# Optimization experiments

Hardware: AMD Instinct MI355X
Metric: run time of the kernel (lower is better)

Reference implementation:

```python
import jax, jax.numpy as jnp
import numpy as np

D_IN = 1024
D_OUT = 1024

def setup_inputs() -> dict:
    key = jax.random.key(0)
    kx, kq, kk, kv = jax.random.split(key, 4)
    X = jax.random.normal(kx, (4, 2048, D_IN), dtype=jnp.float32)
    s = 1.0 / np.sqrt(D_IN)
    Wq = jax.random.uniform(kq, (D_IN, D_OUT), jnp.float32, -s, s)
    Wk = jax.random.uniform(kk, (D_IN, D_OUT), jnp.float32, -s, s)
    Wv = jax.random.uniform(kv, (D_IN, D_OUT), jnp.float32, -s, s)
    return {"X": X, "Wq": Wq, "Wk": Wk, "Wv": Wv}

def reference(X, Wq, Wk, Wv):
    # X: [b, s, d_in]; W*: [d_in, d_out] (torch Linear weight transposed)
    B, S, _ = X.shape
    q = jnp.einsum('bsd,de->bse', X, Wq)
    k = jnp.einsum('bsd,de->bse', X, Wk)
    v = jnp.einsum('bsd,de->bse', X, Wv)
    scores = jnp.einsum('bqe,bke->bqk', q, k)  # [b, s, s]
    causal = jnp.triu(jnp.ones((S, S), dtype=bool), k=1)
    scores = jnp.where(causal, -jnp.inf, scores)
    weights = jax.nn.softmax(scores / jnp.sqrt(jnp.asarray(k.shape[-1], scores.dtype)), axis=-1)
    # dropout p=0.0 (eval) -> identity
    return jnp.einsum('bqk,bke->bqe', weights, v)
```

## Files before the change

### kernel.cpp

```cpp
#include <hip/hip_runtime.h>
#include <cstdint>
#include <cmath>

typedef unsigned short u16;
typedef u16   u16x4  __attribute__((ext_vector_type(4)));
typedef u16   u16x8  __attribute__((ext_vector_type(8)));
typedef __bf16 bf16x8 __attribute__((ext_vector_type(8)));
typedef float f32x4  __attribute__((ext_vector_type(4)));

__device__ __forceinline__ u16 f2bf(float f) {
    uint32_t u = __builtin_bit_cast(uint32_t, f);
    u += 0x7fffu + ((u >> 16) & 1u);
    return (u16)(u >> 16);
}
__device__ __forceinline__ float bf2f(u16 v) {
    uint32_t u = ((uint32_t)v) << 16;
    return __builtin_bit_cast(float, u);
}
__device__ __forceinline__ void gload_lds16(const u16* g, u16* l) {
    __builtin_amdgcn_global_load_lds((const __attribute__((address_space(1))) void*)g,
                                     (__attribute__((address_space(3))) void*)l,
                                     16, 0, 0);
}

__global__ __launch_bounds__(256) void prep_kernel(const float* __restrict__ X,
                                                   const float* __restrict__ Wq,
                                                   const float* __restrict__ Wk,
                                                   const float* __restrict__ Wv,
                                                   u16* __restrict__ Xb,
                                                   u16* __restrict__ Wt) {
    __shared__ u16 tile[64 * 72];
    typedef float f4 __attribute__((ext_vector_type(4)));
    const int bid = blockIdx.x;
    if (bid < 8192) {
        const int idx = bid * 256 + threadIdx.x;
        f4 f = ((const f4*)X)[idx];
        u16x4 o;
        o[0] = f2bf(f[0]); o[1] = f2bf(f[1]); o[2] = f2bf(f[2]); o[3] = f2bf(f[3]);
        ((u16x4*)Xb)[idx] = o;
        return;
    }
    const int id = bid - 8192;
    const int z = id >> 8, rem = id & 255;
    const float* W = (z == 0) ? Wq : (z == 1) ? Wk : Wv;
    u16* out = Wt + ((size_t)z << 20);
    const int nt = (rem & 15) * 64, kt = (rem >> 4) * 64;
    const int t = threadIdx.x, r = t >> 2, cq = (t & 3) * 16;
    const float* src = W + (size_t)(kt + r) * 1024 + nt + cq;
#pragma unroll
    for (int q = 0; q < 4; q++) {
        f4 f = ((const f4*)src)[q];
        tile[r * 72 + cq + q * 4 + 0] = f2bf(f[0]);
        tile[r * 72 + cq + q * 4 + 1] = f2bf(f[1]);
        tile[r * 72 + cq + q * 4 + 2] = f2bf(f[2]);
        tile[r * 72 + cq + q * 4 + 3] = f2bf(f[3]);
    }
    __syncthreads();
    u16x8 o0, o1;
#pragma unroll
    for (int e = 0; e < 8; e++) { o0[e] = tile[(cq + e) * 72 + r]; o1[e] = tile[(cq + 8 + e) * 72 + r]; }
    u16* dst = out + (size_t)(nt + r) * 1024 + kt + cq;
    *(u16x8*)dst = o0;
    *(u16x8*)(dst + 8) = o1;
}

template <int OUTMODE>
__device__ __forceinline__ void gemm_bt_core(u16* __restrict__ smem,
                                             const u16* __restrict__ A,
                                             const u16* __restrict__ Bt,
                                             void* __restrict__ outp,
                                             const int ldk, const int ldo,
                                             const int kbeg, const int kend,
                                             const int m0, const int n0,
                                             const int om0, const int on0) {
    u16* As = smem;
    u16* Bs = smem + 4096;
    const int tid = (int)threadIdx.x;
    const int wave = tid >> 6, lane = tid & 63;
    const int wm = wave >> 1, wn = wave & 1;

    f32x4 acc[4][4] = {};

    const int sr = lane >> 2;
    const int scw = ((lane & 3) ^ ((sr >> 1) & 3)) * 8;
    const u16* gA = A  + (size_t)(m0 + wave * 32 + sr) * ldk + scw;
    const u16* gB = Bt + (size_t)(n0 + wave * 32 + sr) * ldk + scw;
    u16* lA = As + wave * 1024;
    u16* lB = Bs + wave * 1024;
    const size_t rstep = (size_t)ldk * 16;

    const int arow = lane & 15;
    const int ksw  = (arow >> 1) & 3;
    const int koff = (((lane >> 4) ^ ksw)) * 8;
    const u16* pa = As + (wm * 64 + arow) * 32 + koff;
    const u16* pb = Bs + (wn * 64 + arow) * 32 + koff;

    for (int k0 = kbeg; k0 < kend; k0 += 32) {
        gload_lds16(gA + k0,         lA);
        gload_lds16(gA + k0 + rstep, lA + 512);
        gload_lds16(gB + k0,         lB);
        gload_lds16(gB + k0 + rstep, lB + 512);
        __syncthreads();
        bf16x8 a[4], b[4];
#pragma unroll
        for (int i = 0; i < 4; i++) a[i] = *(const bf16x8*)(pa + i * 512);
#pragma unroll
        for (int j = 0; j < 4; j++) b[j] = *(const bf16x8*)(pb + j * 512);
#pragma unroll
        for (int i = 0; i < 4; i++)
#pragma unroll
            for (int j = 0; j < 4; j++)
                acc[i][j] = __builtin_amdgcn_mfma_f32_16x16x32_bf16(a[i], b[j], acc[i][j], 0, 0, 0);
        __syncthreads();
    }

    const int row0 = om0 + wm * 64 + ((lane >> 4) << 2);
    const int col0 = on0 + wn * 64 + (lane & 15);
    if constexpr (OUTMODE == 0) {
        u16* o = (u16*)outp;
#pragma unroll
        for (int i = 0; i < 4; i++)
#pragma unroll
            for (int r = 0; r < 4; r++) {
                u16* po = o + (size_t)(row0 + i * 16 + r) * ldo + col0;
#pragma unroll
                for (int j = 0; j < 4; j++) po[j * 16] = f2bf(acc[i][j][r]);
            }
    } else {
        float* o = (float*)outp;
#pragma unroll
        for (int i = 0; i < 4; i++)
#pragma unroll
            for (int r = 0; r < 4; r++) {
                float* po = o + (size_t)(row0 + i * 16 + r) * ldo + col0;
#pragma unroll
                for (int j = 0; j < 4; j++) po[j * 16] = acc[i][j][r];
            }
    }
}

__global__ __launch_bounds__(512, 2) void qkv_gemm_kernel(const u16* __restrict__ Xb,
                                                          const u16* __restrict__ Wt,
                                                          u16* __restrict__ QKV) {
    __shared__ u16 lds[49152];
    const int bid = blockIdx.x;
    const int xcd = bid & 7, slot = bid >> 3;
    const int z = slot >> 5, r32 = slot & 31;
    const int m0 = (xcd * 4 + (r32 >> 3)) << 8;
    const int n0 = (r32 & 7) << 7;

    const u16* __restrict__ A = Xb;
    const u16* __restrict__ B = Wt + ((size_t)z << 20);
    u16* __restrict__ C = QKV + ((size_t)z << 23);

    const int tid = (int)threadIdx.x;
    const int w = tid >> 6, l = tid & 63;
    const int wm = w >> 2, wn = w & 3;

    const int srow = w * 16 + (l >> 3);
    const int scol = ((l & 7) ^ ((l >> 3) & 7)) * 8;
    const u16* gA = A + (size_t)(m0 + srow) * 1024 + scol;
    const u16* gB = B + (size_t)(n0 + srow) * 1024 + scol;
    u16* const sA = lds + w * 1024;
    u16* const sB = lds + 32768 + w * 1024;

    const int c0 = ((l >> 4) ^ (l & 7)) * 8;
    const u16* const pa_ = lds + (wm * 64 + (l & 15)) * 64;
    const u16* const pb_ = lds + 32768 + (wn * 32 + (l & 15)) * 64;

    f32x4 acc[2][4][2] = {};
    bf16x8 a[4][2], b[2][2];

#define MFMA_ __builtin_amdgcn_mfma_f32_16x16x32_bf16
#define STG_A(BUF, H, T) \
    gload_lds16(gA + (size_t)((H) * 128) * 1024 + (T) * 64,       sA + (BUF) + (H) * 8192); \
    gload_lds16(gA + (size_t)((H) * 128 + 8) * 1024 + (T) * 64,   sA + (BUF) + (H) * 8192 + 512);
#define STG_B(BUF, T) \
    gload_lds16(gB + (T) * 64,                                    sB + ((BUF) >> 1)); \
    gload_lds16(gB + (size_t)8 * 1024 + (T) * 64,                 sB + ((BUF) >> 1) + 512);
#define LD_A(BUF, QA) \
    _Pragma("unroll") for (int m_ = 0; m_ < 4; m_++) { \
        a[m_][0] = *(const bf16x8*)(pa_ + (BUF) + (QA) * 8192 + m_ * 1024 + c0); \
        a[m_][1] = *(const bf16x8*)(pa_ + (BUF) + (QA) * 8192 + m_ * 1024 + (c0 ^ 32)); \
    }
#define LD_B(BUF) \
    _Pragma("unroll") for (int n_ = 0; n_ < 2; n_++) { \
        b[n_][0] = *(const bf16x8*)(pb_ + ((BUF) >> 1) + n_ * 1024 + c0); \
        b[n_][1] = *(const bf16x8*)(pb_ + ((BUF) >> 1) + n_ * 1024 + (c0 ^ 32)); \
    }
#define MM(QA) \
    _Pragma("unroll") for (int m_ = 0; m_ < 4; m_++) { \
        _Pragma("unroll") for (int n_ = 0; n_ < 2; n_++) { \
            acc[QA][m_][n_] = MFMA_(a[m_][0], b[n_][0], acc[QA][m_][n_], 0, 0, 0); \
            acc[QA][m_][n_] = MFMA_(a[m_][1], b[n_][1], acc[QA][m_][n_], 0, 0, 0); \
        } \
    }
#define VM6 asm volatile("s_waitcnt vmcnt(6)" ::: "memory");
#define VM2 asm volatile("s_waitcnt vmcnt(2)" ::: "memory");
#define VM0 asm volatile("s_waitcnt vmcnt(0)" ::: "memory");
#define VMN
#define BAR __builtin_amdgcn_s_barrier();
#define PRIO1 __builtin_amdgcn_s_setprio(1);
#define PRIO0 __builtin_amdgcn_s_setprio(0);
#define TILE(BUF, OBUF, T1, S1, T2, S2, VMA, VMB) \
    LD_A(BUF, 0) LD_B(BUF) \
    if (S1) { STG_A(OBUF, 1, T1) } \
    VMA BAR PRIO1 MM(0) PRIO0 BAR \
    LD_A(BUF, 1) \
    if (S2) { STG_A(BUF, 0, T2) STG_B(BUF, T2) } \
    VMB BAR PRIO1 MM(1) PRIO0 BAR

    STG_A(0, 0, 0) STG_B(0, 0) STG_A(0, 1, 0)
    STG_A(16384, 0, 1) STG_B(16384, 1)
    asm volatile("s_waitcnt vmcnt(6)" ::: "memory");
    __builtin_amdgcn_s_barrier();

#pragma unroll 1
    for (int i = 0; i < 7; ++i) {
        const int t1 = 2 * i + 1, t2 = 2 * i + 2, t3 = 2 * i + 3;
        TILE(0,     16384, t1, 1, t2, 1, VM6, VM6)
        TILE(16384, 0,     t2, 1, t3, 1, VM6, VM6)
    }
    TILE(0,     16384, 15, 1, 0, 0, VM6, VM2)
    TILE(16384, 0,     0,  0, 0, 0, VM0, VMN)

    const int row0 = m0 + wm * 64 + ((l >> 4) << 2);
    const int col0 = n0 + wn * 32 + (l & 15);
#pragma unroll
    for (int qa = 0; qa < 2; qa++)
#pragma unroll
        for (int m = 0; m < 4; m++)
#pragma unroll
            for (int r = 0; r < 4; r++) {
                u16* po = C + (size_t)(row0 + qa * 128 + m * 16 + r) * 1024 + col0;
#pragma unroll
                for (int n = 0; n < 2; n++) po[n * 16] = f2bf(acc[qa][m][n][r]);
            }
#undef MFMA_
#undef STG_A
#undef STG_B
#undef LD_A
#undef LD_B
#undef MM
#undef VM6
#undef VM2
#undef VM0
#undef VMN
#undef BAR
#undef PRIO1
#undef PRIO0
#undef TILE
}

__global__ __launch_bounds__(256) void s_tr_kernel(const u16* __restrict__ QKV,
                                                   u16* __restrict__ S,
                                                   u16* __restrict__ Vt) {
    __shared__ u16 smem[8192];
    const int bid = blockIdx.x;
    if (bid < 576) {
        const int xcd = bid & 7, slot = bid >> 3;
        const int b = xcd >> 1, half = xcd & 1;
        int it = half ? 11 : 0;
        const int ntiles = half ? 70 : 66;
        if (slot >= ntiles) return;
        int acc = 0;
        while (acc + it + 1 <= slot) { acc += it + 1; it++; }
        const int jt = slot - acc;
        const u16* Q  = QKV + ((size_t)b << 21);
        const u16* Kp = QKV + ((size_t)1 << 23) + ((size_t)b << 21);
        gemm_bt_core<0>(smem, Q, Kp, S + ((size_t)b << 22), 1024, 2048, 0, 1024,
                        it * 128, jt * 128, it * 128, jt * 128);
        return;
    }
    const int id = bid - 576;
    const int z = id >> 9, rem = id & 511;
    const u16* src = QKV + ((size_t)2 << 23) + ((size_t)z << 21);
    u16* dst = Vt + ((size_t)z << 21);
    const int st = (rem & 31) * 64, et = (rem >> 5) * 64;
    u16 (*tile)[72] = (u16(*)[72])smem;
    const int t = threadIdx.x, r = t >> 2, cq = (t & 3) * 16;
    const u16* p = src + (size_t)(st + r) * 1024 + et + cq;
    u16x8 u0 = *(const u16x8*)p;
    u16x8 u1 = *(const u16x8*)(p + 8);
#pragma unroll
    for (int e = 0; e < 8; e++) { tile[r][cq + e] = u0[e]; tile[r][cq + 8 + e] = u1[e]; }
    __syncthreads();
    u16x8 o0, o1;
#pragma unroll
    for (int e = 0; e < 8; e++) { o0[e] = tile[cq + e][r]; o1[e] = tile[cq + 8 + e][r]; }
    u16* q = dst + (size_t)(et + r) * 2048 + st + cq;
    *(u16x8*)q = o0;
    *(u16x8*)(q + 8) = o1;
}

__global__ __launch_bounds__(256) void pv_gemm_kernel(const u16* __restrict__ P,
                                                      const u16* __restrict__ Vt,
                                                      float* __restrict__ O,
                                                      float* __restrict__ Part) {
    __shared__ u16 smem[8192];
    const unsigned char IT[24]   = {15,14, 7,14,13,13,12,12, 15, 6,11,11,10,10, 9, 5,  0, 1, 2, 8, 3, 9, 8, 4};
    const unsigned char KIND[24] = { 1, 1, 0, 2, 1, 2, 1, 2,  2, 0, 1, 2, 1, 2, 1, 0,  0, 0, 0, 2, 0, 2, 1, 0};
    const int j = blockIdx.x;
    const int slot = j >> 5, combo = j & 31;
    const int it = IT[slot], kind = KIND[slot];
    const int b = combo >> 3, n0 = (combo & 7) * 128;
    const int u = it + 1, h = (u + 1) >> 1;
    const int k_lo = (kind == 2) ? h * 128 : 0;
    const int k_hi = (kind == 1) ? h * 128 : u * 128;
    if (kind == 2) {
        float* dst = Part + ((size_t)((it - 8) * 32 + combo) << 14);
        gemm_bt_core<1>(smem, P + ((size_t)b << 22), Vt + ((size_t)b << 21), dst,
                        2048, 128, k_lo, k_hi, it * 128, n0, 0, 0);
    } else {
        gemm_bt_core<1>(smem, P + ((size_t)b << 22), Vt + ((size_t)b << 21),
                        O + ((size_t)b << 21),
                        2048, 1024, k_lo, k_hi, it * 128, n0, it * 128, n0);
    }
}

__global__ __launch_bounds__(256) void reduce_kernel(float* __restrict__ O,
                                                     const float* __restrict__ Part) {
    const int t = blockIdx.x;
    const int tile = t >> 2, q = t & 3;
    const int it = 8 + (tile >> 5), combo = tile & 31;
    const int b = combo >> 3, n0 = (combo & 7) * 128;
    const f32x4* p = (const f32x4*)(Part + ((size_t)tile << 14)) + q * 1024;
    float* o = O + ((size_t)b << 21) + (size_t)(it * 128 + q * 32) * 1024 + n0;
    const int tid = threadIdx.x;
#pragma unroll
    for (int e = 0; e < 4; e++) {
        const int flat = e * 256 + tid;
        const int row = flat >> 5, col = (flat & 31) * 4;
        f32x4 pv = p[flat];
        f32x4* po = (f32x4*)(o + (size_t)row * 1024 + col);
        f32x4 ov = *po;
        ov[0] += pv[0]; ov[1] += pv[1]; ov[2] += pv[2]; ov[3] += pv[3];
        *po = ov;
    }
}

__global__ __launch_bounds__(256) void softmax_kernel(u16* __restrict__ S) {
    const int wave = threadIdx.x >> 6, lane = threadIdx.x & 63;
    const int g = blockIdx.x * 4 + wave;
    const int b = g >> 11, i = g & 2047;
    u16* row = S + ((size_t)b << 22) + ((size_t)i << 11);
    const int n = i + 1;
    const int kend = ((i >> 7) + 1) << 7;
    const int nt_ = (kend + 511) >> 9;
    const float NEG = -1e30f;
    float v[32];
    float m = NEG;
#pragma unroll
    for (int t = 0; t < 4; t++) {
        if (t < nt_) {
            u16x8 u = *(const u16x8*)(row + t * 512 + lane * 8);
#pragma unroll
            for (int e = 0; e < 8; e++) {
                const int col = t * 512 + lane * 8 + e;
                float f = (col < n) ? bf2f(u[e]) : NEG;
                v[t * 8 + e] = f;
                m = fmaxf(m, f);
            }
        }
    }
#pragma unroll
    for (int off = 32; off > 0; off >>= 1) m = fmaxf(m, __shfl_xor(m, off, 64));
    const float sc = 0.03125f * 1.44269504088896f;
    float s = 0.f;
#pragma unroll
    for (int t = 0; t < 4; t++) {
        if (t < nt_) {
#pragma unroll
            for (int e = 0; e < 8; e++) {
                const float x = v[t * 8 + e];
                const float e2 = (x == NEG) ? 0.f : exp2f((x - m) * sc);
                v[t * 8 + e] = e2;
                s += e2;
            }
        }
    }
#pragma unroll
    for (int off = 32; off > 0; off >>= 1) s += __shfl_xor(s, off, 64);
    const float inv = 1.f / s;
#pragma unroll
    for (int t = 0; t < 4; t++) {
        if (t < nt_) {
            u16x8 o;
#pragma unroll
            for (int e = 0; e < 8; e++) o[e] = f2bf(v[t * 8 + e] * inv);
            *(u16x8*)(row + t * 512 + lane * 8) = o;
        }
    }
}

extern "C" void kernel_launch(void* const* d_in, const int* in_sizes, int n_in,
                              void* d_out, int out_size, void* d_ws, size_t ws_size,
                              hipStream_t stream) {
    const float* X  = (const float*)d_in[0];
    const float* Wq = (const float*)d_in[1];
    const float* Wk = (const float*)d_in[2];
    const float* Wv = (const float*)d_in[3];
    float* out = (float*)d_out;

    u16* ws  = (u16*)d_ws;
    u16* Xb  = ws;
    u16* Wt  = Xb + ((size_t)1 << 23);
    u16* QKV = Wt + 3 * ((size_t)1 << 20);
    u16* S   = QKV + 3 * ((size_t)1 << 23);
    u16* Vt  = Xb;
    float* Part = (float*)QKV;

    prep_kernel<<<8960, 256, 0, stream>>>(X, Wq, Wk, Wv, Xb, Wt);
    qkv_gemm_kernel<<<768, 512, 0, stream>>>(Xb, Wt, QKV);
    s_tr_kernel<<<2624, 256, 0, stream>>>(QKV, S, Vt);
    softmax_kernel<<<2048, 256, 0, stream>>>(S);
    pv_gemm_kernel<<<768, 256, 0, stream>>>(S, Vt, out, Part);
    reduce_kernel<<<1024, 256, 0, stream>>>(out, Part);
}
```

Baseline: 237.6 us.

## Drop split-K partials and reduce kernel; pair short and long PV tiles

The PV GEMM no longer splits long causal row tiles into two K halves written to a partial buffer and summed by a separate reduce kernel. Each of 512 blocks now computes a full causal K range for one output tile. The grid is ordered so the first half covers short row tiles and the second half covers long ones in reverse, so a CU that finishes early picks up a long tile and per-CU work stays balanced. This removes the partial-buffer traffic and one kernel launch, but it relies on the dynamic block scheduler to actually pair short and long tiles.

```diff
diff --git a/kernel.cpp b/kernel.cpp
--- a/kernel.cpp
+++ b/kernel.cpp
@@ -295,48 +295,16 @@
 
 __global__ __launch_bounds__(256) void pv_gemm_kernel(const u16* __restrict__ P,
                                                       const u16* __restrict__ Vt,
-                                                      float* __restrict__ O,
-                                                      float* __restrict__ Part) {
+                                                      float* __restrict__ O) {
     __shared__ u16 smem[8192];
-    const unsigned char IT[24]   = {15,14, 7,14,13,13,12,12, 15, 6,11,11,10,10, 9, 5,  0, 1, 2, 8, 3, 9, 8, 4};
-    const unsigned char KIND[24] = { 1, 1, 0, 2, 1, 2, 1, 2,  2, 0, 1, 2, 1, 2, 1, 0,  0, 0, 0, 2, 0, 2, 1, 0};
     const int j = blockIdx.x;
-    const int slot = j >> 5, combo = j & 31;
-    const int it = IT[slot], kind = KIND[slot];
+    const int phase = j >> 8, c = j & 255;
+    const int slot = c >> 5, combo = c & 31;
+    const int it = phase ? (15 - slot) : slot;
     const int b = combo >> 3, n0 = (combo & 7) * 128;
-    const int u = it + 1, h = (u + 1) >> 1;
-    const int k_lo = (kind == 2) ? h * 128 : 0;
-    const int k_hi = (kind == 1) ? h * 128 : u * 128;
-    if (kind == 2) {
-        float* dst = Part + ((size_t)((it - 8) * 32 + combo) << 14);
-        gemm_bt_core<1>(smem, P + ((size_t)b << 22), Vt + ((size_t)b << 21), dst,
-                        2048, 128, k_lo, k_hi, it * 128, n0, 0, 0);
-    } else {
-        gemm_bt_core<1>(smem, P + ((size_t)b << 22), Vt + ((size_t)b << 21),
-                        O + ((size_t)b << 21),
-                        2048, 1024, k_lo, k_hi, it * 128, n0, it * 128, n0);
-    }
-}
-
-__global__ __launch_bounds__(256) void reduce_kernel(float* __restrict__ O,
-                                                     const float* __restrict__ Part) {
-    const int t = blockIdx.x;
-    const int tile = t >> 2, q = t & 3;
-    const int it = 8 + (tile >> 5), combo = tile & 31;
-    const int b = combo >> 3, n0 = (combo & 7) * 128;
-    const f32x4* p = (const f32x4*)(Part + ((size_t)tile << 14)) + q * 1024;
-    float* o = O + ((size_t)b << 21) + (size_t)(it * 128 + q * 32) * 1024 + n0;
-    const int tid = threadIdx.x;
-#pragma unroll
-    for (int e = 0; e < 4; e++) {
-        const int flat = e * 256 + tid;
-        const int row = flat >> 5, col = (flat & 31) * 4;
-        f32x4 pv = p[flat];
-        f32x4* po = (f32x4*)(o + (size_t)row * 1024 + col);
-        f32x4 ov = *po;
-        ov[0] += pv[0]; ov[1] += pv[1]; ov[2] += pv[2]; ov[3] += pv[3];
-        *po = ov;
-    }
+    gemm_bt_core<1>(smem, P + ((size_t)b << 22), Vt + ((size_t)b << 21),
+                    O + ((size_t)b << 21),
+                    2048, 1024, 0, (it + 1) * 128, it * 128, n0, it * 128, n0);
 }
 
 __global__ __launch_bounds__(256) void softmax_kernel(u16* __restrict__ S) {
@@ -408,12 +376,10 @@
     u16* QKV = Wt + 3 * ((size_t)1 << 20);
     u16* S   = QKV + 3 * ((size_t)1 << 23);
     u16* Vt  = Xb;
-    float* Part = (float*)QKV;
 
     prep_kernel<<<8960, 256, 0, stream>>>(X, Wq, Wk, Wv, Xb, Wt);
     qkv_gemm_kernel<<<768, 512, 0, stream>>>(Xb, Wt, QKV);
     s_tr_kernel<<<2624, 256, 0, stream>>>(QKV, S, Vt);
     softmax_kernel<<<2048, 256, 0, stream>>>(S);
-    pv_gemm_kernel<<<768, 256, 0, stream>>>(S, Vt, out, Part);
-    reduce_kernel<<<1024, 256, 0, stream>>>(out, Part);
-}
+    pv_gemm_kernel<<<512, 256, 0, stream>>>(S, Vt, out);
+}
```

Measured after the change: 239.3 us. Within noise of the previous version (+0.7%).
